# Optimization experiments

Hardware: AMD Instinct MI355X
Metric: run time of the kernel (lower is better)

The kernel has to match this reference:

```python
import jax, jax.numpy as jnp
import numpy as np

VOCAB, E, H, OUT = 32000, 128, 128, 16
N, L = 8192, 32


def setup_inputs() -> dict:
    key = jax.random.key(0)
    ks = jax.random.split(key, 12)
    s_lstm = 1.0 / np.sqrt(H)
    s_g1 = 1.0 / np.sqrt(2 * H)
    s_g2 = 1.0 / np.sqrt(OUT)
    return {
        "tokens": jax.random.randint(ks[0], (N, L), 0, VOCAB, dtype=jnp.int64)
        if jax.config.read("jax_enable_x64") else jax.random.randint(ks[0], (N, L), 0, VOCAB, dtype=jnp.int32),
        "adj": jax.random.uniform(ks[1], (N, N), dtype=jnp.float32) / N,
        "embed_W": jax.random.normal(ks[2], (VOCAB, E), dtype=jnp.float32),
        "W_ih": jax.random.uniform(ks[3], (4 * H, E), jnp.float32, -s_lstm, s_lstm),
        "W_hh": jax.random.uniform(ks[4], (4 * H, H), jnp.float32, -s_lstm, s_lstm),
        "b_ih": jax.random.uniform(ks[5], (4 * H,), jnp.float32, -s_lstm, s_lstm),
        "b_hh": jax.random.uniform(ks[6], (4 * H,), jnp.float32, -s_lstm, s_lstm),
        "gc1_W": jax.random.uniform(ks[7], (H, 2 * H), jnp.float32, -s_g1, s_g1),
        "gc1_b": jax.random.uniform(ks[8], (2 * H,), jnp.float32, -s_g1, s_g1),
        "gc2_W": jax.random.uniform(ks[9], (2 * H, OUT), jnp.float32, -s_g2, s_g2),
        "gc2_b": jax.random.uniform(ks[10], (OUT,), jnp.float32, -s_g2, s_g2),
    }


def _lstm_final_h(x, W_ih, W_hh, b_ih, b_hh):
    # x: [N, L, E] -> final hidden state [N, H] (torch gate order i,f,g,o)
    Hd = W_hh.shape[1]
    # precompute input projections for all timesteps: [L, N, 4H]
    xi = jnp.einsum('nle,ge->lng', x, W_ih) + b_ih + b_hh

    def step(carry, xt):
        h, c = carry
        gates = xt + h @ W_hh.T
        i, f, g, o = jnp.split(gates, 4, axis=-1)
        i, f, o = jax.nn.sigmoid(i), jax.nn.sigmoid(f), jax.nn.sigmoid(o)
        g = jnp.tanh(g)
        c = f * c + i * g
        h = o * jnp.tanh(c)
        return (h, c), None

    n = x.shape[0]
    h0 = jnp.zeros((n, Hd), x.dtype)
    (h, _), _ = jax.lax.scan(step, (h0, h0), xi)
    return h


def reference(tokens, adj, embed_W, W_ih, W_hh, b_ih, b_hh, gc1_W, gc1_b, gc2_W, gc2_b):
    x = embed_W[tokens]                                  # [N, L, E]
    feat = _lstm_final_h(x, W_ih, W_hh, b_ih, b_hh)      # [N, H]
    h1 = jax.nn.relu(adj @ (feat @ gc1_W) + gc1_b)       # [N, 2H]
    logits = adj @ (h1 @ gc2_W) + gc2_b                  # [N, OUT]
    return jax.nn.log_softmax(logits, axis=1)
```

## Files before the change

### kernel.cpp

```cpp
#include <hip/hip_runtime.h>

typedef __attribute__((ext_vector_type(8))) short bf16x8;
typedef __attribute__((ext_vector_type(4))) float f32x4;

__device__ __forceinline__ short f2bf(float f){
  union { float f; unsigned u; } v; v.f = f;
  unsigned r = v.u + 0x7fffu + ((v.u >> 16) & 1u);
  return (short)(r >> 16);
}
__device__ __forceinline__ bf16x8 pack8(float4 a, float4 b){
  bf16x8 v;
  v[0]=f2bf(a.x); v[1]=f2bf(a.y); v[2]=f2bf(a.z); v[3]=f2bf(a.w);
  v[4]=f2bf(b.x); v[5]=f2bf(b.y); v[6]=f2bf(b.z); v[7]=f2bf(b.w);
  return v;
}
__device__ __forceinline__ f32x4 mfma16(bf16x8 a, bf16x8 b, f32x4 c){
  return __builtin_amdgcn_mfma_f32_16x16x32_bf16(a, b, c, 0, 0, 0);
}
__device__ __forceinline__ float sigm(float x){
  return __builtin_amdgcn_rcpf(1.f + __expf(-x));
}
__device__ __forceinline__ float tanh_(float x){
  return 1.f - 2.f*__builtin_amdgcn_rcpf(1.f + __expf(2.f*x));
}

__global__ __launch_bounds__(512) void lstm_kernel(
    const int* __restrict__ tokens, const float* __restrict__ embed,
    const float* __restrict__ Wih, const float* __restrict__ Whh,
    const float* __restrict__ bih, const float* __restrict__ bhh,
    float* __restrict__ feat)
{
  __shared__ short hbuf[32*128];
  const int tid  = threadIdx.x;
  const int wave = tid >> 6, lane = tid & 63;
  const int l15  = lane & 15, lhi = lane >> 4;
  const int nbase = blockIdx.x * 32;
  const int ucol  = wave*16 + l15;

  bf16x8 wihf[4][4], whhf[4][4];
  for(int g=0; g<4; ++g){
    const float* wi = Wih + (size_t)(g*128 + ucol)*128;
    const float* wh = Whh + (size_t)(g*128 + ucol)*128;
    #pragma unroll
    for(int kt=0; kt<4; ++kt){
      int e0 = kt*32 + lhi*8;
      float4 a0 = *(const float4*)(wi+e0), a1 = *(const float4*)(wi+e0+4);
      float4 b0 = *(const float4*)(wh+e0), b1 = *(const float4*)(wh+e0+4);
      wihf[g][kt] = pack8(a0,a1);
      whhf[g][kt] = pack8(b0,b1);
    }
  }
  float bs[4];
  #pragma unroll
  for(int g=0; g<4; ++g) bs[g] = bih[g*128+ucol] + bhh[g*128+ucol];

  float c[2][4], hreg[2][4];
  #pragma unroll
  for(int m=0;m<2;++m) for(int r=0;r<4;++r){ c[m][r]=0.f; hreg[m][r]=0.f; }

  for(int i=tid; i<32*128; i+=512) hbuf[i]=0;
  __syncthreads();

  const int trow0 = nbase + l15;
  const int trow1 = nbase + 16 + l15;

  for(int l=0; l<32; ++l){
    f32x4 acc[2][4];
    #pragma unroll
    for(int m=0;m<2;++m) for(int g=0;g<4;++g) acc[m][g]=(f32x4){0.f,0.f,0.f,0.f};

    int tok0 = tokens[trow0*32 + l];
    int tok1 = tokens[trow1*32 + l];
    const float* e0 = embed + (size_t)tok0*128;
    const float* e1 = embed + (size_t)tok1*128;
    bf16x8 xa[2][4];
    #pragma unroll
    for(int kt=0; kt<4; ++kt){
      int k0 = kt*32 + lhi*8;
      float4 u0=*(const float4*)(e0+k0), u1=*(const float4*)(e0+k0+4);
      float4 v0=*(const float4*)(e1+k0), v1=*(const float4*)(e1+k0+4);
      xa[0][kt]=pack8(u0,u1);
      xa[1][kt]=pack8(v0,v1);
    }
    #pragma unroll
    for(int kt=0; kt<4; ++kt){
      int sbyte = kt*64 + lhi*16;
      int r0 = l15, r1 = 16 + l15;
      int a0 = (r0*256 + sbyte) ^ ((r0&7)<<4);
      int a1 = (r1*256 + sbyte) ^ ((r1&7)<<4);
      bf16x8 h0 = *(const bf16x8*)((const char*)hbuf + a0);
      bf16x8 h1 = *(const bf16x8*)((const char*)hbuf + a1);
      #pragma unroll
      for(int g=0; g<4; ++g){
        acc[0][g]=mfma16(h0, whhf[g][kt], acc[0][g]);
        acc[1][g]=mfma16(h1, whhf[g][kt], acc[1][g]);
      }
      #pragma unroll
      for(int g=0; g<4; ++g){
        acc[0][g]=mfma16(xa[0][kt], wihf[g][kt], acc[0][g]);
        acc[1][g]=mfma16(xa[1][kt], wihf[g][kt], acc[1][g]);
      }
    }
    __syncthreads();
    #pragma unroll
    for(int m=0;m<2;++m){
      #pragma unroll
      for(int r=0;r<4;++r){
        float gi = acc[m][0][r] + bs[0];
        float gf = acc[m][1][r] + bs[1];
        float gg = acc[m][2][r] + bs[2];
        float go = acc[m][3][r] + bs[3];
        float i_ = sigm(gi), f_ = sigm(gf), o_ = sigm(go), g_ = tanh_(gg);
        float cc = f_*c[m][r] + i_*g_;
        c[m][r] = cc;
        float hh = o_*tanh_(cc);
        hreg[m][r] = hh;
        int row = m*16 + lhi*4 + r;
        int wb = (row*256 + ucol*2) ^ ((row&7)<<4);
        *(short*)((char*)hbuf + wb) = f2bf(hh);
      }
    }
    __syncthreads();
  }
  #pragma unroll
  for(int m=0;m<2;++m) for(int r=0;r<4;++r){
    int row = nbase + m*16 + lhi*4 + r;
    feat[(size_t)row*128 + ucol] = hreg[m][r];
  }
}

__global__ __launch_bounds__(256) void gc1_kernel(
  const float* __restrict__ feat, const float* __restrict__ W1,
  short* __restrict__ Y1t)
{
  __shared__ float fs[128][36];
  int tid = threadIdx.x; int nb = blockIdx.x*32;
  #pragma unroll
  for(int i=0;i<4;++i){
    int idx = i*256 + tid;
    float4 v = ((const float4*)(feat + (size_t)nb*128))[idx];
    int n = idx>>5, k0 = (idx&31)*4;
    fs[k0][n]=v.x; fs[k0+1][n]=v.y; fs[k0+2][n]=v.z; fs[k0+3][n]=v.w;
  }
  __syncthreads();
  float acc[32];
  #pragma unroll
  for(int n=0;n<32;++n) acc[n]=0.f;
  int j = tid;
  for(int k=0;k<128;++k){
    float w = W1[k*256 + j];
    #pragma unroll
    for(int n4=0;n4<8;++n4){
      float4 f = *(const float4*)&fs[k][n4*4];
      acc[n4*4+0]+=f.x*w; acc[n4*4+1]+=f.y*w; acc[n4*4+2]+=f.z*w; acc[n4*4+3]+=f.w*w;
    }
  }
  unsigned* dst = (unsigned*)(Y1t + (size_t)j*8192 + nb);
  #pragma unroll
  for(int n=0;n<16;++n){
    unsigned lo = (unsigned short)f2bf(acc[2*n]);
    unsigned hi = (unsigned short)f2bf(acc[2*n+1]);
    dst[n] = lo | (hi<<16);
  }
}

__global__ __launch_bounds__(256) void gemm1_kernel(
  const float* __restrict__ adj, const short* __restrict__ Y1t,
  float* __restrict__ part)
{
  __shared__ short As[64*40];
  int tid=threadIdx.x, lane=tid&63, wid=tid>>6;
  int wr=wid>>1, wc=wid&1, l15=lane&15, lhi=lane>>4;
  int rb=(blockIdx.x>>2)*64;
  int ks=blockIdx.x&3;
  size_t kb0=(size_t)ks*2048;
  f32x4 acc[2][8];
  #pragma unroll
  for(int m=0;m<2;++m) for(int n=0;n<8;++n) acc[m][n]=(f32x4){0.f,0.f,0.f,0.f};
  int arow=tid>>2, aq=tid&3;
  const float* asrc = adj + (size_t)(rb+arow)*8192 + kb0 + aq*8;
  short* adst = As + arow*40 + aq*8;
  for(int kt=0; kt<64; ++kt){
    float4 f0=((const float4*)asrc)[0], f1=((const float4*)asrc)[1];
    __syncthreads();
    *(bf16x8*)adst = pack8(f0,f1);
    __syncthreads();
    bf16x8 af[2];
    #pragma unroll
    for(int m=0;m<2;++m)
      af[m] = *(const bf16x8*)(As + (wr*32+m*16+l15)*40 + lhi*8);
    const short* yb = Y1t + kb0 + kt*32 + lhi*8;
    #pragma unroll
    for(int n=0;n<8;++n){
      bf16x8 bf_ = *(const bf16x8*)(yb + (size_t)(wc*128+n*16+l15)*8192);
      #pragma unroll
      for(int m=0;m<2;++m) acc[m][n]=mfma16(af[m], bf_, acc[m][n]);
    }
    asrc += 32;
  }
  float* pb = part + ((size_t)ks*8192 + rb)*256;
  #pragma unroll
  for(int m=0;m<2;++m) for(int n=0;n<8;++n){
    int row0=wr*32+m*16+lhi*4, col=wc*128+n*16+l15;
    #pragma unroll
    for(int r=0;r<4;++r) pb[(size_t)(row0+r)*256+col]=acc[m][n][r];
  }
}

__global__ __launch_bounds__(256) void reduce_kernel(
  const float* __restrict__ part, const float* __restrict__ b1,
  const float* __restrict__ W2, float* __restrict__ Y2)
{
  __shared__ float h1s[8][256];
  __shared__ float w2s[256*16];
  int tid=threadIdx.x, rb=blockIdx.x*8;
  for(int i=tid;i<1024;i+=256) ((float4*)w2s)[i]=((const float4*)W2)[i];
  int r=tid>>5, cb=(tid&31)*8;
  const float* p0 = part + (size_t)(rb+r)*256 + cb;
  float a[8];
  #pragma unroll
  for(int q=0;q<8;++q) a[q]=0.f;
  #pragma unroll
  for(int ks=0;ks<4;++ks){
    const float* p = p0 + (size_t)ks*2097152;
    float4 u=((const float4*)p)[0], v=((const float4*)p)[1];
    a[0]+=u.x; a[1]+=u.y; a[2]+=u.z; a[3]+=u.w;
    a[4]+=v.x; a[5]+=v.y; a[6]+=v.z; a[7]+=v.w;
  }
  #pragma unroll
  for(int q=0;q<8;++q){
    float v = a[q] + b1[cb+q];
    h1s[r][cb+q] = v>0.f ? v : 0.f;
  }
  __syncthreads();
  if(tid<128){
    int rr=tid>>4, j=tid&15;
    float s=0.f;
    for(int k4=0;k4<64;++k4){
      float4 h = *(const float4*)&h1s[rr][k4*4];
      s += h.x*w2s[(k4*4+0)*16+j] + h.y*w2s[(k4*4+1)*16+j]
         + h.z*w2s[(k4*4+2)*16+j] + h.w*w2s[(k4*4+3)*16+j];
    }
    Y2[(size_t)(rb+rr)*16+j]=s;
  }
}

__global__ __launch_bounds__(256) void gemm2_kernel(
  const float* __restrict__ adj, const float* __restrict__ Y2,
  const float* __restrict__ b2, float* __restrict__ out)
{
  __shared__ float y2t[16][516];
  __shared__ float red[16][16][16];
  int tid=threadIdx.x;
  int rb=blockIdx.x*16;
  int r=tid>>4, st=tid&15;
  float acc[16];
  #pragma unroll
  for(int j=0;j<16;++j) acc[j]=0.f;
  int sj = tid&15, skb = tid>>4;
  for(int kc=0;kc<16;++kc){
    __syncthreads();
    const float* ysrc = Y2 + (size_t)(kc*512)*16;
    for(int kk=0;kk<32;++kk){
      int k = skb*32 + kk;
      y2t[sj][k] = ysrc[k*16 + sj];
    }
    __syncthreads();
    const float* arow = adj + (size_t)(rb+r)*8192 + kc*512 + st*4;
    #pragma unroll
    for(int i=0;i<8;++i){
      float4 av = *(const float4*)(arow + i*64);
      int k = st*4 + i*64;
      #pragma unroll
      for(int j=0;j<16;++j){
        float4 y = *(const float4*)&y2t[j][k];
        acc[j] += av.x*y.x + av.y*y.y + av.z*y.z + av.w*y.w;
      }
    }
  }
  #pragma unroll
  for(int j=0;j<16;++j) red[r][j][st]=acc[j];
  __syncthreads();
  int r2=tid>>4, j=tid&15;
  float s=0.f;
  #pragma unroll
  for(int q=0;q<16;q+=4){
    float4 v = *(const float4*)&red[r2][j][q];
    s += v.x+v.y+v.z+v.w;
  }
  float logit = s + b2[j];
  float m = logit;
  for(int msk=8;msk;msk>>=1) m = fmaxf(m, __shfl_xor(m, msk, 16));
  float e = __expf(logit - m);
  float den = e;
  for(int msk=8;msk;msk>>=1) den += __shfl_xor(den, msk, 16);
  out[(size_t)(rb+r2)*16 + j] = logit - m - __logf(den);
}

extern "C" void kernel_launch(void* const* d_in, const int* in_sizes, int n_in,
                              void* d_out, int out_size, void* d_ws, size_t ws_size,
                              hipStream_t stream) {
  const int*   tokens = (const int*)d_in[0];
  const float* adj    = (const float*)d_in[1];
  const float* embed  = (const float*)d_in[2];
  const float* Wih    = (const float*)d_in[3];
  const float* Whh    = (const float*)d_in[4];
  const float* bih    = (const float*)d_in[5];
  const float* bhh    = (const float*)d_in[6];
  const float* W1     = (const float*)d_in[7];
  const float* b1     = (const float*)d_in[8];
  const float* W2     = (const float*)d_in[9];
  const float* b2     = (const float*)d_in[10];
  float* out = (float*)d_out;

  char* ws = (char*)d_ws;
  float* feat = (float*)ws;
  short* Y1t  = (short*)(ws + (4u<<20));
  float* part = (float*)(ws + (8u<<20));
  float* Y2   = (float*)(ws + (40u<<20));

  lstm_kernel  <<<dim3(256),  dim3(512), 0, stream>>>(tokens, embed, Wih, Whh, bih, bhh, feat);
  gc1_kernel   <<<dim3(256),  dim3(256), 0, stream>>>(feat, W1, Y1t);
  gemm1_kernel <<<dim3(512),  dim3(256), 0, stream>>>(adj, Y1t, part);
  reduce_kernel<<<dim3(1024), dim3(256), 0, stream>>>(part, b1, W2, Y2);
  gemm2_kernel <<<dim3(512),  dim3(256), 0, stream>>>(adj, Y2, b2, out);
}
```

Baseline: 839.9 us.

## Pipeline LSTM embedding loads, retile adj GEMM, restructure second adj pass

The LSTM kernel now stages tokens in LDS and prefetches the next timestep's embedding rows into a double-buffered swizzled LDS tile. It also double-buffers the hidden state, which removes one barrier per step. gemm1 moves to 128x128 tiles with 512 threads, loads 128-wide K chunks into a double-buffered LDS tile, and prefetches the next chunk into registers. gemm2 drops the transposed LDS staging of Y2: each wave handles 4 rows, streams adj directly, reads Y2 from global/L2, and reduces across lanes with shuffles. The trade-off is higher register pressure and a larger LDS footprint per block.

New measurement: 759.6 us. -9.6%, faster.

```diff
diff --git a/kernel.cpp b/kernel.cpp
--- a/kernel.cpp
+++ b/kernel.cpp
@@ -24,13 +24,15 @@
   return 1.f - 2.f*__builtin_amdgcn_rcpf(1.f + __expf(2.f*x));
 }
 
-__global__ __launch_bounds__(512) void lstm_kernel(
+__global__ __launch_bounds__(512,2) void lstm_kernel(
     const int* __restrict__ tokens, const float* __restrict__ embed,
     const float* __restrict__ Wih, const float* __restrict__ Whh,
     const float* __restrict__ bih, const float* __restrict__ bhh,
     float* __restrict__ feat)
 {
-  __shared__ short hbuf[32*128];
+  __shared__ short hbuf[2*32*128];
+  __shared__ short xbuf[2*32*128];
+  __shared__ int   tokbuf[32*32];
   const int tid  = threadIdx.x;
   const int wave = tid >> 6, lane = tid & 63;
   const int l15  = lane & 15, lhi = lane >> 4;
@@ -38,6 +40,7 @@
   const int ucol  = wave*16 + l15;
 
   bf16x8 wihf[4][4], whhf[4][4];
+  #pragma unroll
   for(int g=0; g<4; ++g){
     const float* wi = Wih + (size_t)(g*128 + ucol)*128;
     const float* wh = Whh + (size_t)(g*128 + ucol)*128;
@@ -54,54 +57,57 @@
   #pragma unroll
   for(int g=0; g<4; ++g) bs[g] = bih[g*128+ucol] + bhh[g*128+ucol];
 
+  for(int i=tid; i<1024; i+=512) tokbuf[i] = tokens[(size_t)nbase*32 + i];
+
   float c[2][4], hreg[2][4];
   #pragma unroll
   for(int m=0;m<2;++m) for(int r=0;r<4;++r){ c[m][r]=0.f; hreg[m][r]=0.f; }
 
-  for(int i=tid; i<32*128; i+=512) hbuf[i]=0;
-  __syncthreads();
-
-  const int trow0 = nbase + l15;
-  const int trow1 = nbase + 16 + l15;
-
+  *(bf16x8*)((char*)hbuf + tid*16) = (bf16x8){0,0,0,0,0,0,0,0};
+  __syncthreads();
+
+  const int srow = tid >> 4, sseg = tid & 15;
+  {
+    int tok = tokbuf[srow*32 + 0];
+    const float* e = embed + (size_t)tok*128 + sseg*8;
+    float4 a = *(const float4*)e, b = *(const float4*)(e+4);
+    int byte = (srow*256 + sseg*16) ^ ((srow&7)<<4);
+    *(bf16x8*)((char*)xbuf + byte) = pack8(a,b);
+  }
+  __syncthreads();
+
+  float4 sa, sb;
+  #pragma unroll 1
   for(int l=0; l<32; ++l){
+    if(l < 31){
+      int tok = tokbuf[srow*32 + l + 1];
+      const float* e = embed + (size_t)tok*128 + sseg*8;
+      sa = *(const float4*)e; sb = *(const float4*)(e+4);
+    }
+    const char* hb = (const char*)hbuf + (l&1)*8192;
+    const char* xb = (const char*)xbuf + (l&1)*8192;
     f32x4 acc[2][4];
     #pragma unroll
     for(int m=0;m<2;++m) for(int g=0;g<4;++g) acc[m][g]=(f32x4){0.f,0.f,0.f,0.f};
-
-    int tok0 = tokens[trow0*32 + l];
-    int tok1 = tokens[trow1*32 + l];
-    const float* e0 = embed + (size_t)tok0*128;
-    const float* e1 = embed + (size_t)tok1*128;
-    bf16x8 xa[2][4];
     #pragma unroll
     for(int kt=0; kt<4; ++kt){
-      int k0 = kt*32 + lhi*8;
-      float4 u0=*(const float4*)(e0+k0), u1=*(const float4*)(e0+k0+4);
-      float4 v0=*(const float4*)(e1+k0), v1=*(const float4*)(e1+k0+4);
-      xa[0][kt]=pack8(u0,u1);
-      xa[1][kt]=pack8(v0,v1);
-    }
-    #pragma unroll
-    for(int kt=0; kt<4; ++kt){
-      int sbyte = kt*64 + lhi*16;
-      int r0 = l15, r1 = 16 + l15;
-      int a0 = (r0*256 + sbyte) ^ ((r0&7)<<4);
-      int a1 = (r1*256 + sbyte) ^ ((r1&7)<<4);
-      bf16x8 h0 = *(const bf16x8*)((const char*)hbuf + a0);
-      bf16x8 h1 = *(const bf16x8*)((const char*)hbuf + a1);
+      int cbyte = kt*64 + lhi*16;
+      int swz = (l15&7)<<4;
+      int a0 = (l15*256 + cbyte) ^ swz;
+      int a1 = ((16+l15)*256 + cbyte) ^ swz;
+      bf16x8 h0 = *(const bf16x8*)(hb + a0);
+      bf16x8 h1 = *(const bf16x8*)(hb + a1);
+      bf16x8 x0 = *(const bf16x8*)(xb + a0);
+      bf16x8 x1 = *(const bf16x8*)(xb + a1);
       #pragma unroll
       for(int g=0; g<4; ++g){
         acc[0][g]=mfma16(h0, whhf[g][kt], acc[0][g]);
         acc[1][g]=mfma16(h1, whhf[g][kt], acc[1][g]);
-      }
-      #pragma unroll
-      for(int g=0; g<4; ++g){
-        acc[0][g]=mfma16(xa[0][kt], wihf[g][kt], acc[0][g]);
-        acc[1][g]=mfma16(xa[1][kt], wihf[g][kt], acc[1][g]);
-      }
-    }
-    __syncthreads();
+        acc[0][g]=mfma16(x0, wihf[g][kt], acc[0][g]);
+        acc[1][g]=mfma16(x1, wihf[g][kt], acc[1][g]);
+      }
+    }
+    char* hn = (char*)hbuf + ((l+1)&1)*8192;
     #pragma unroll
     for(int m=0;m<2;++m){
       #pragma unroll
@@ -117,8 +123,12 @@
         hreg[m][r] = hh;
         int row = m*16 + lhi*4 + r;
         int wb = (row*256 + ucol*2) ^ ((row&7)<<4);
-        *(short*)((char*)hbuf + wb) = f2bf(hh);
-      }
+        *(short*)(hn + wb) = f2bf(hh);
+      }
+    }
+    if(l < 31){
+      int byte = ((l+1)&1)*8192 + ((srow*256 + sseg*16) ^ ((srow&7)<<4));
+      *(bf16x8*)((char*)xbuf + byte) = pack8(sa,sb);
     }
     __syncthreads();
   }
@@ -164,46 +174,68 @@
   }
 }
 
-__global__ __launch_bounds__(256) void gemm1_kernel(
+__global__ __launch_bounds__(512,2) void gemm1_kernel(
   const float* __restrict__ adj, const short* __restrict__ Y1t,
   float* __restrict__ part)
 {
-  __shared__ short As[64*40];
+  __shared__ short As[2*128*128];
   int tid=threadIdx.x, lane=tid&63, wid=tid>>6;
-  int wr=wid>>1, wc=wid&1, l15=lane&15, lhi=lane>>4;
-  int rb=(blockIdx.x>>2)*64;
+  int wr=wid>>2, wc=wid&3, l15=lane&15, lhi=lane>>4;
+  int rb=(blockIdx.x>>2)*128;
   int ks=blockIdx.x&3;
   size_t kb0=(size_t)ks*2048;
-  f32x4 acc[2][8];
-  #pragma unroll
-  for(int m=0;m<2;++m) for(int n=0;n<8;++n) acc[m][n]=(f32x4){0.f,0.f,0.f,0.f};
-  int arow=tid>>2, aq=tid&3;
-  const float* asrc = adj + (size_t)(rb+arow)*8192 + kb0 + aq*8;
-  short* adst = As + arow*40 + aq*8;
-  for(int kt=0; kt<64; ++kt){
-    float4 f0=((const float4*)asrc)[0], f1=((const float4*)asrc)[1];
+  f32x4 acc[4][4];
+  #pragma unroll
+  for(int m=0;m<4;++m) for(int n=0;n<4;++n) acc[m][n]=(f32x4){0.f,0.f,0.f,0.f};
+
+  const int srow = tid>>2, sseg = tid&3;
+  const float* asrc = adj + (size_t)(rb+srow)*8192 + kb0 + sseg*32;
+  float4 r[8];
+  {
+    const float4* p = (const float4*)asrc;
+    #pragma unroll
+    for(int i=0;i<8;++i) r[i]=p[i];
+  }
+  #pragma unroll 1
+  for(int t=0; t<16; ++t){
+    char* dst = (char*)As + (t&1)*32768;
+    #pragma unroll
+    for(int q=0;q<4;++q){
+      int byte = (srow*256 + (sseg*32+q*8)*2) ^ ((srow&7)<<4);
+      *(bf16x8*)(dst + byte) = pack8(r[2*q], r[2*q+1]);
+    }
     __syncthreads();
-    *(bf16x8*)adst = pack8(f0,f1);
+    if(t<15){
+      const float4* p = (const float4*)(asrc + (t+1)*128);
+      #pragma unroll
+      for(int i=0;i<8;++i) r[i]=p[i];
+    }
+    const char* cur = (const char*)As + (t&1)*32768;
+    #pragma unroll
+    for(int kk=0;kk<4;++kk){
+      bf16x8 af[4];
+      #pragma unroll
+      for(int m=0;m<4;++m){
+        int row = wr*64 + m*16 + l15;
+        int byte = (row*256 + (kk*32+lhi*8)*2) ^ ((row&7)<<4);
+        af[m] = *(const bf16x8*)(cur + byte);
+      }
+      const short* yb = Y1t + kb0 + t*128 + kk*32 + lhi*8;
+      #pragma unroll
+      for(int n=0;n<4;++n){
+        bf16x8 bfr = *(const bf16x8*)(yb + (size_t)(wc*64 + n*16 + l15)*8192);
+        #pragma unroll
+        for(int m=0;m<4;++m) acc[m][n]=mfma16(af[m], bfr, acc[m][n]);
+      }
+    }
     __syncthreads();
-    bf16x8 af[2];
-    #pragma unroll
-    for(int m=0;m<2;++m)
-      af[m] = *(const bf16x8*)(As + (wr*32+m*16+l15)*40 + lhi*8);
-    const short* yb = Y1t + kb0 + kt*32 + lhi*8;
-    #pragma unroll
-    for(int n=0;n<8;++n){
-      bf16x8 bf_ = *(const bf16x8*)(yb + (size_t)(wc*128+n*16+l15)*8192);
-      #pragma unroll
-      for(int m=0;m<2;++m) acc[m][n]=mfma16(af[m], bf_, acc[m][n]);
-    }
-    asrc += 32;
   }
   float* pb = part + ((size_t)ks*8192 + rb)*256;
   #pragma unroll
-  for(int m=0;m<2;++m) for(int n=0;n<8;++n){
-    int row0=wr*32+m*16+lhi*4, col=wc*128+n*16+l15;
-    #pragma unroll
-    for(int r=0;r<4;++r) pb[(size_t)(row0+r)*256+col]=acc[m][n][r];
+  for(int m=0;m<4;++m) for(int n=0;n<4;++n){
+    int row0=wr*64+m*16+lhi*4, col=wc*64+n*16+l15;
+    #pragma unroll
+    for(int q=0;q<4;++q) pb[(size_t)(row0+q)*256+col]=acc[m][n][q];
   }
 }
 
@@ -249,46 +281,52 @@
   const float* __restrict__ adj, const float* __restrict__ Y2,
   const float* __restrict__ b2, float* __restrict__ out)
 {
-  __shared__ float y2t[16][516];
-  __shared__ float red[16][16][16];
-  int tid=threadIdx.x;
+  __shared__ float red[16][16];
+  int tid=threadIdx.x, lane=tid&63, w=tid>>6;
   int rb=blockIdx.x*16;
-  int r=tid>>4, st=tid&15;
-  float acc[16];
-  #pragma unroll
-  for(int j=0;j<16;++j) acc[j]=0.f;
-  int sj = tid&15, skb = tid>>4;
-  for(int kc=0;kc<16;++kc){
-    __syncthreads();
-    const float* ysrc = Y2 + (size_t)(kc*512)*16;
-    for(int kk=0;kk<32;++kk){
-      int k = skb*32 + kk;
-      y2t[sj][k] = ysrc[k*16 + sj];
-    }
-    __syncthreads();
-    const float* arow = adj + (size_t)(rb+r)*8192 + kc*512 + st*4;
-    #pragma unroll
-    for(int i=0;i<8;++i){
-      float4 av = *(const float4*)(arow + i*64);
-      int k = st*4 + i*64;
-      #pragma unroll
-      for(int j=0;j<16;++j){
-        float4 y = *(const float4*)&y2t[j][k];
-        acc[j] += av.x*y.x + av.y*y.y + av.z*y.z + av.w*y.w;
-      }
-    }
-  }
-  #pragma unroll
-  for(int j=0;j<16;++j) red[r][j][st]=acc[j];
+  int rowb=rb + w*4;
+  float acc[4][16];
+  #pragma unroll
+  for(int rr=0;rr<4;++rr) for(int j=0;j<16;++j) acc[rr][j]=0.f;
+  const float* a0 = adj + (size_t)rowb*8192;
+  #pragma unroll 1
+  for(int it=0; it<32; ++it){
+    int kb = it*256 + lane*4;
+    float4 av[4];
+    #pragma unroll
+    for(int rr=0;rr<4;++rr) av[rr] = *(const float4*)(a0 + (size_t)rr*8192 + kb);
+    #pragma unroll
+    for(int kk=0;kk<4;++kk){
+      const float* yr = Y2 + (size_t)(kb+kk)*16;
+      float4 y0=*(const float4*)yr,      y1=*(const float4*)(yr+4);
+      float4 y2v=*(const float4*)(yr+8), y3=*(const float4*)(yr+12);
+      #pragma unroll
+      for(int rr=0;rr<4;++rr){
+        float a = (kk==0)?av[rr].x:(kk==1)?av[rr].y:(kk==2)?av[rr].z:av[rr].w;
+        acc[rr][0] +=a*y0.x;  acc[rr][1] +=a*y0.y;  acc[rr][2] +=a*y0.z;  acc[rr][3] +=a*y0.w;
+        acc[rr][4] +=a*y1.x;  acc[rr][5] +=a*y1.y;  acc[rr][6] +=a*y1.z;  acc[rr][7] +=a*y1.w;
+        acc[rr][8] +=a*y2v.x; acc[rr][9] +=a*y2v.y; acc[rr][10]+=a*y2v.z; acc[rr][11]+=a*y2v.w;
+        acc[rr][12]+=a*y3.x;  acc[rr][13]+=a*y3.y;  acc[rr][14]+=a*y3.z;  acc[rr][15]+=a*y3.w;
+      }
+    }
+  }
+  #pragma unroll
+  for(int mask=32; mask; mask>>=1){
+    #pragma unroll
+    for(int rr=0;rr<4;++rr)
+      #pragma unroll
+      for(int j=0;j<16;++j)
+        acc[rr][j] += __shfl_xor(acc[rr][j], mask);
+  }
+  if(lane==0){
+    #pragma unroll
+    for(int rr=0;rr<4;++rr)
+      #pragma unroll
+      for(int j=0;j<16;++j) red[w*4+rr][j]=acc[rr][j];
+  }
   __syncthreads();
   int r2=tid>>4, j=tid&15;
-  float s=0.f;
-  #pragma unroll
-  for(int q=0;q<16;q+=4){
-    float4 v = *(const float4*)&red[r2][j][q];
-    s += v.x+v.y+v.z+v.w;
-  }
-  float logit = s + b2[j];
+  float logit = red[r2][j] + b2[j];
   float m = logit;
   for(int msk=8;msk;msk>>=1) m = fmaxf(m, __shfl_xor(m, msk, 16));
   float e = __expf(logit - m);
@@ -321,7 +359,7 @@
 
   lstm_kernel  <<<dim3(256),  dim3(512), 0, stream>>>(tokens, embed, Wih, Whh, bih, bhh, feat);
   gc1_kernel   <<<dim3(256),  dim3(256), 0, stream>>>(feat, W1, Y1t);
-  gemm1_kernel <<<dim3(512),  dim3(256), 0, stream>>>(adj, Y1t, part);
+  gemm1_kernel <<<dim3(256),  dim3(512), 0, stream>>>(adj, Y1t, part);
   reduce_kernel<<<dim3(1024), dim3(256), 0, stream>>>(part, b1, W2, Y2);
   gemm2_kernel <<<dim3(512),  dim3(256), 0, stream>>>(adj, Y2, b2, out);
 }
```
